# Optimization experiments

Hardware: AMD Instinct MI355X
Metric: run time of the kernel (lower is better)

## Reference

```python
import jax, jax.numpy as jnp
import numpy as np

N_NODES = 50000
N_EDGES = 800000
IN_F = 128
HEADS = 8
HEAD_DIM = 16
ALPHA = 0.2  # LeakyReLU negative slope
EPS = 1e-6


def setup_inputs() -> dict:
    key = jax.random.key(0)
    k1, k2, k3, k4 = jax.random.split(key, 4)
    x = jax.random.normal(k1, (N_NODES, IN_F), dtype=jnp.float32)
    edge_index = jax.random.randint(k2, (2, N_EDGES), 0, N_NODES, dtype=jnp.int32)
    std = 1.0 / np.sqrt(IN_F)
    W = jax.random.uniform(k3, (HEADS, IN_F, HEAD_DIM), minval=-std, maxval=std, dtype=jnp.float32)
    a = jax.random.uniform(k4, (HEADS, 2 * HEAD_DIM, 1), minval=-std, maxval=std, dtype=jnp.float32)
    bias = jnp.zeros((HEADS * HEAD_DIM,), dtype=jnp.float32)
    return {"x": x, "edge_index": edge_index, "W": W, "a": a, "bias": bias}


def reference(x, edge_index, W, a, bias):
    N = x.shape[0]
    src = edge_index[0]
    tgt = edge_index[1]
    # per-head linear transform: [N, H, D]
    h = jnp.einsum('nf,hfd->nhd', x, W)
    # split attention vector: a = [a_src; a_tgt], each [H, D]
    a_src = a[:, :HEAD_DIM, 0]
    a_tgt = a[:, HEAD_DIM:, 0]
    # node-level partial scores, then gather (equivalent to concat@a on edges)
    s_node_src = jnp.einsum('nhd,hd->nh', h, a_src)  # [N, H]
    s_node_tgt = jnp.einsum('nhd,hd->nh', h, a_tgt)  # [N, H]
    scores = s_node_src[src] + s_node_tgt[tgt]       # [E, H]
    scores = jnp.where(scores >= 0, scores, ALPHA * scores)  # LeakyReLU
    # edge softmax per target node, per head (global max subtract + clamp, as in source)
    max_per_head = jnp.max(scores, axis=0, keepdims=True)    # [1, H]
    exp_scores = jnp.exp(jnp.clip(scores - max_per_head, -20.0, 20.0))  # [E, H]
    denom = jax.ops.segment_sum(exp_scores, tgt, num_segments=N) + EPS  # [N, H]
    attn = exp_scores / denom[tgt]                                      # [E, H]
    # weighted scatter-add aggregation
    weighted = h[src] * attn[:, :, None]                                # [E, H, D]
    agg = jax.ops.segment_sum(weighted, tgt, num_segments=N)            # [N, H, D]
    out = agg.reshape(N, HEADS * HEAD_DIM) + bias
    return out
```

## Files before the change

### kernel.cpp

```cpp
#include <hip/hip_runtime.h>
#include <stdint.h>

#define N_NODES 50000
#define N_EDGES 800000
#define IN_F 128
#define HEADS 8
#define HEAD_DIM 16
#define ALPHA 0.2f
#define EPSV 1e-6f

#define NB 196
#define CAP 4800

typedef short short8 __attribute__((ext_vector_type(8)));
typedef float floatx4 __attribute__((ext_vector_type(4)));

__device__ __forceinline__ float bflo(unsigned v) {
    return __uint_as_float(v << 16);
}
__device__ __forceinline__ float bfhi(unsigned v) {
    return __uint_as_float(v & 0xffff0000u);
}
__device__ __forceinline__ unsigned f2bf(float f) {
    unsigned u = __float_as_uint(f);
    return (u + 0x7fffu + ((u >> 16) & 1u)) >> 16;
}

__global__ __launch_bounds__(256) void k_wt(const float* __restrict__ W,
                                            const float* __restrict__ a,
                                            ushort* __restrict__ WTb,
                                            ushort* __restrict__ WSb,
                                            int* __restrict__ gcnt) {
    int b = blockIdx.x, t = threadIdx.x;
    if (b == 64) {
        for (int i = t; i < 2048; i += 256) {
            int j = i >> 7, f = i & 127;
            int h = j >> 1;
            const float* wrow = W + h * 2048 + f * 16;
            const float* arow = a + h * 32 + (j & 1) * 16;
            float ssum = 0.f;
#pragma unroll
            for (int d = 0; d < 16; d++) ssum = fmaf(wrow[d], arow[d], ssum);
            WSb[i] = (ushort)f2bf(ssum);
        }
        return;
    }
    int i = b * 256 + t;
    int c = i >> 7, f = i & 127;
    WTb[i] = (ushort)f2bf(W[(c >> 4) * 2048 + f * 16 + (c & 15)]);
    if (i < NB) gcnt[i] = 0;
}

__global__ __launch_bounds__(256) void k_mid(const float* __restrict__ x,
                                             const ushort* __restrict__ WTb,
                                             const ushort* __restrict__ WSb,
                                             ushort* __restrict__ hb,
                                             float* __restrict__ sst,
                                             const int* __restrict__ srcA,
                                             const int* __restrict__ tgtA,
                                             int* __restrict__ gcnt,
                                             unsigned* __restrict__ bucketbuf) {
    int bi = blockIdx.x;
    int q3 = bi / 3, r3 = bi - q3 * 3;
    int t = threadIdx.x;

    if (r3 == 2) {
        __shared__ int lcnt[NB];
        __shared__ int lbase[NB];
        if (t < NB) lcnt[t] = 0;
        __syncthreads();

        int base = q3 * 2048 + t;
        int tg[8], sr[8];
        bool vld[8];
#pragma unroll
        for (int k = 0; k < 8; k++) {
            int e = base + k * 256;
            vld[k] = (e < N_EDGES);
            int ee = vld[k] ? e : 0;
            tg[k] = tgtA[ee];
            sr[k] = srcA[ee];
        }
#pragma unroll
        for (int k = 0; k < 8; k++)
            if (vld[k]) atomicAdd(&lcnt[tg[k] >> 8], 1);
        __syncthreads();
        if (t < NB) {
            int c = lcnt[t];
            lbase[t] = (c > 0) ? atomicAdd(&gcnt[t], c) : 0;
            lcnt[t] = 0;
        }
        __syncthreads();
#pragma unroll
        for (int k = 0; k < 8; k++) {
            if (vld[k]) {
                int b = tg[k] >> 8;
                int off = atomicAdd(&lcnt[b], 1);
                int pos = lbase[b] + off;
                if (pos < CAP)
                    bucketbuf[(size_t)b * CAP + pos] =
                        ((unsigned)(tg[k] & 255) << 16) | (unsigned)sr[k];
            }
        }
        return;
    }

    int mb = q3 * 2 + r3;
    int wave = t >> 6, lane = t & 63;
    int quad = lane >> 4, col = lane & 15;
    int nb = mb * 64 + wave * 16;

    int na = nb + col;
    int nac = na < N_NODES ? na : (N_NODES - 1);
    const float* xrow = x + (size_t)nac * 128 + quad * 8;

    floatx4 acc[8];
    floatx4 z = {0.f, 0.f, 0.f, 0.f};
#pragma unroll
    for (int ct = 0; ct < 8; ct++) acc[ct] = z;
    floatx4 accS = z;

#pragma unroll
    for (int kc = 0; kc < 4; kc++) {
        float4 f0 = *(const float4*)(xrow + kc * 32);
        float4 f1 = *(const float4*)(xrow + kc * 32 + 4);
        short8 af;
        af[0] = (short)f2bf(f0.x); af[1] = (short)f2bf(f0.y);
        af[2] = (short)f2bf(f0.z); af[3] = (short)f2bf(f0.w);
        af[4] = (short)f2bf(f1.x); af[5] = (short)f2bf(f1.y);
        af[6] = (short)f2bf(f1.z); af[7] = (short)f2bf(f1.w);
#pragma unroll
        for (int ct = 0; ct < 8; ct++) {
            const ushort* wrow = WTb + (size_t)(ct * 16 + col) * 128 + kc * 32 + quad * 8;
            short8 bf = *(const short8*)wrow;
            acc[ct] = __builtin_amdgcn_mfma_f32_16x16x32_bf16(af, bf, acc[ct], 0, 0, 0);
        }
        const ushort* srow = WSb + (size_t)col * 128 + kc * 32 + quad * 8;
        short8 bs = *(const short8*)srow;
        accS = __builtin_amdgcn_mfma_f32_16x16x32_bf16(af, bs, accS, 0, 0, 0);
    }

#pragma unroll
    for (int r = 0; r < 4; r++) {
        int node = nb + quad * 4 + r;
        bool nv = (node < N_NODES);
        if (nv) {
            ushort* hrow = hb + (size_t)node * 128 + col;
#pragma unroll
            for (int ct = 0; ct < 8; ct++)
                hrow[ct * 16] = (ushort)f2bf(acc[ct][r]);
            sst[(size_t)node * 16 + col] = accS[r];
        }
    }
}

__global__ __launch_bounds__(512) void k_passB(const unsigned* __restrict__ bucketbuf,
                                               const int* __restrict__ gcnt,
                                               int* __restrict__ rowptr,
                                               ushort* __restrict__ src16) {
    __shared__ int bin[256];
    __shared__ int wsum[4];
    __shared__ int woff[4];
    __shared__ int sbase;
    __shared__ ushort stage[CAP];
    int t = threadIdx.x, lane = t & 63, w = t >> 6;
    int b = blockIdx.x;

    if (t < 256) bin[t] = 0;

    int g = (t < NB) ? gcnt[t] : 0;
    int incg = g;
#pragma unroll
    for (int off = 1; off < 64; off <<= 1) {
        int nn = __shfl_up(incg, off, 64);
        if (lane >= off) incg += nn;
    }
    if (t < 256 && lane == 63) wsum[w] = incg;
    __syncthreads();
    if (t == 0) {
        woff[0] = 0;
        woff[1] = wsum[0];
        woff[2] = wsum[0] + wsum[1];
        woff[3] = wsum[0] + wsum[1] + wsum[2];
    }
    __syncthreads();
    if (t == b) sbase = woff[w] + incg - g;
    if (b == 0 && t == 0) rowptr[N_NODES] = N_EDGES;
    __syncthreads();
    int base = sbase;
    int n = gcnt[b]; if (n > CAP) n = CAP;
    const unsigned* buf = bucketbuf + (size_t)b * CAP;

    for (int i = t; i < n; i += 512)
        atomicAdd(&bin[buf[i] >> 16], 1);
    __syncthreads();
    int v = (t < 256) ? bin[t] : 0;
    int inc = v;
#pragma unroll
    for (int off = 1; off < 64; off <<= 1) {
        int nn = __shfl_up(inc, off, 64);
        if (lane >= off) inc += nn;
    }
    if (t < 256 && lane == 63) wsum[w] = inc;
    __syncthreads();
    if (t == 0) {
        woff[0] = 0;
        woff[1] = wsum[0];
        woff[2] = wsum[0] + wsum[1];
        woff[3] = wsum[0] + wsum[1] + wsum[2];
    }
    __syncthreads();
    if (t < 256) {
        int excl = woff[w] + inc - v;
        int node = b * 256 + t;
        if (node < N_NODES) rowptr[node] = base + excl;
        __syncthreads();
        bin[t] = excl;
    } else {
        __syncthreads();
    }
    __syncthreads();
    for (int i = t; i < n; i += 512) {
        unsigned p = buf[i];
        int off = atomicAdd(&bin[p >> 16], 1);
        stage[off] = (ushort)(p & 0xffffu);
    }
    __syncthreads();
    for (int i = t; i < n; i += 512)
        src16[base + i] = stage[i];
}

__global__ __launch_bounds__(256) void k_fused(const int* __restrict__ rowptr,
                                               const ushort* __restrict__ src16,
                                               const float* __restrict__ sst,
                                               const unsigned* __restrict__ h16,
                                               const float* __restrict__ bias,
                                               float* __restrict__ outb) {
    int t = threadIdx.x;
    int wave = t >> 6, lane = t & 63;
    int half = lane >> 5, hl = lane & 31;
    int n = blockIdx.x * 8 + wave * 2 + half;
    int head = hl >> 2;
    int hh = head * 2;
    int c = 4 * hl;

    const uint2* h2 = (const uint2*)h16;

    float st = sst[n * 16 + hh + 1];
    int begin = rowptr[n], end = rowptr[n + 1];

    float ax = 0.f, ay = 0.f, az = 0.f, aw = 0.f, den = 0.f;
    int e = begin;
    int nfull = (end - begin) >> 3;
    int s0, s1, s2, s3, s4, s5, s6, s7;
    if (nfull > 0) {
        s0 = src16[e];     s1 = src16[e + 1];
        s2 = src16[e + 2]; s3 = src16[e + 3];
        s4 = src16[e + 4]; s5 = src16[e + 5];
        s6 = src16[e + 6]; s7 = src16[e + 7];
    }
    for (int it = 0; it < nfull; ++it) {
        int c0 = s0, c1 = s1, c2 = s2, c3 = s3;
        int c4 = s4, c5 = s5, c6 = s6, c7 = s7;
        int en = e + 8;
        if (it + 1 < nfull) {
            s0 = src16[en];     s1 = src16[en + 1];
            s2 = src16[en + 2]; s3 = src16[en + 3];
            s4 = src16[en + 4]; s5 = src16[en + 5];
            s6 = src16[en + 6]; s7 = src16[en + 7];
        }
        float t0 = sst[c0 * 16 + hh];
        float t1 = sst[c1 * 16 + hh];
        float t2 = sst[c2 * 16 + hh];
        float t3 = sst[c3 * 16 + hh];
        float t4 = sst[c4 * 16 + hh];
        float t5 = sst[c5 * 16 + hh];
        float t6 = sst[c6 * 16 + hh];
        float t7 = sst[c7 * 16 + hh];
        uint2 p0 = h2[c0 * 32 + hl];
        uint2 p1 = h2[c1 * 32 + hl];
        uint2 p2 = h2[c2 * 32 + hl];
        uint2 p3 = h2[c3 * 32 + hl];
        uint2 p4 = h2[c4 * 32 + hl];
        uint2 p5 = h2[c5 * 32 + hl];
        uint2 p6 = h2[c6 * 32 + hl];
        uint2 p7 = h2[c7 * 32 + hl];
        float v0 = t0 + st; v0 = v0 >= 0.f ? v0 : ALPHA * v0;
        float v1 = t1 + st; v1 = v1 >= 0.f ? v1 : ALPHA * v1;
        float v2 = t2 + st; v2 = v2 >= 0.f ? v2 : ALPHA * v2;
        float v3 = t3 + st; v3 = v3 >= 0.f ? v3 : ALPHA * v3;
        float v4 = t4 + st; v4 = v4 >= 0.f ? v4 : ALPHA * v4;
        float v5 = t5 + st; v5 = v5 >= 0.f ? v5 : ALPHA * v5;
        float v6 = t6 + st; v6 = v6 >= 0.f ? v6 : ALPHA * v6;
        float v7 = t7 + st; v7 = v7 >= 0.f ? v7 : ALPHA * v7;
        float x0 = __expf(v0);
        float x1 = __expf(v1);
        float x2 = __expf(v2);
        float x3 = __expf(v3);
        float x4 = __expf(v4);
        float x5 = __expf(v5);
        float x6 = __expf(v6);
        float x7 = __expf(v7);
        den += ((x0 + x1) + (x2 + x3)) + ((x4 + x5) + (x6 + x7));
        ax = fmaf(x0, bflo(p0.x), fmaf(x1, bflo(p1.x), fmaf(x2, bflo(p2.x), fmaf(x3, bflo(p3.x), ax))));
        ax = fmaf(x4, bflo(p4.x), fmaf(x5, bflo(p5.x), fmaf(x6, bflo(p6.x), fmaf(x7, bflo(p7.x), ax))));
        ay = fmaf(x0, bfhi(p0.x), fmaf(x1, bfhi(p1.x), fmaf(x2, bfhi(p2.x), fmaf(x3, bfhi(p3.x), ay))));
        ay = fmaf(x4, bfhi(p4.x), fmaf(x5, bfhi(p5.x), fmaf(x6, bfhi(p6.x), fmaf(x7, bfhi(p7.x), ay))));
        az = fmaf(x0, bflo(p0.y), fmaf(x1, bflo(p1.y), fmaf(x2, bflo(p2.y), fmaf(x3, bflo(p3.y), az))));
        az = fmaf(x4, bflo(p4.y), fmaf(x5, bflo(p5.y), fmaf(x6, bflo(p6.y), fmaf(x7, bflo(p7.y), az))));
        aw = fmaf(x0, bfhi(p0.y), fmaf(x1, bfhi(p1.y), fmaf(x2, bfhi(p2.y), fmaf(x3, bfhi(p3.y), aw))));
        aw = fmaf(x4, bfhi(p4.y), fmaf(x5, bfhi(p5.y), fmaf(x6, bfhi(p6.y), fmaf(x7, bfhi(p7.y), aw))));
        e = en;
    }
    if (e + 3 < end) {
        int c0 = src16[e];
        int c1 = src16[e + 1];
        int c2 = src16[e + 2];
        int c3 = src16[e + 3];
        float t0 = sst[c0 * 16 + hh];
        float t1 = sst[c1 * 16 + hh];
        float t2 = sst[c2 * 16 + hh];
        float t3 = sst[c3 * 16 + hh];
        uint2 p0 = h2[c0 * 32 + hl];
        uint2 p1 = h2[c1 * 32 + hl];
        uint2 p2 = h2[c2 * 32 + hl];
        uint2 p3 = h2[c3 * 32 + hl];
        float v0 = t0 + st; v0 = v0 >= 0.f ? v0 : ALPHA * v0;
        float v1 = t1 + st; v1 = v1 >= 0.f ? v1 : ALPHA * v1;
        float v2 = t2 + st; v2 = v2 >= 0.f ? v2 : ALPHA * v2;
        float v3 = t3 + st; v3 = v3 >= 0.f ? v3 : ALPHA * v3;
        float x0 = __expf(v0);
        float x1 = __expf(v1);
        float x2 = __expf(v2);
        float x3 = __expf(v3);
        den += (x0 + x1) + (x2 + x3);
        ax = fmaf(x0, bflo(p0.x), fmaf(x1, bflo(p1.x), fmaf(x2, bflo(p2.x), fmaf(x3, bflo(p3.x), ax))));
        ay = fmaf(x0, bfhi(p0.x), fmaf(x1, bfhi(p1.x), fmaf(x2, bfhi(p2.x), fmaf(x3, bfhi(p3.x), ay))));
        az = fmaf(x0, bflo(p0.y), fmaf(x1, bflo(p1.y), fmaf(x2, bflo(p2.y), fmaf(x3, bflo(p3.y), az))));
        aw = fmaf(x0, bfhi(p0.y), fmaf(x1, bfhi(p1.y), fmaf(x2, bfhi(p2.y), fmaf(x3, bfhi(p3.y), aw))));
        e += 4;
    }
    for (; e < end; e++) {
        int sA = src16[e];
        float ssA = sst[sA * 16 + hh];
        uint2 pA = h2[sA * 32 + hl];
        float vA = ssA + st; vA = vA >= 0.f ? vA : ALPHA * vA;
        float exA = __expf(vA);
        den += exA;
        ax = fmaf(exA, bflo(pA.x), ax);
        ay = fmaf(exA, bfhi(pA.x), ay);
        az = fmaf(exA, bflo(pA.y), az);
        aw = fmaf(exA, bfhi(pA.y), aw);
    }
    float r = 1.f / (den + EPSV);
    float4 b = *(const float4*)(bias + c);
    float4 o;
    o.x = fmaf(ax, r, b.x);
    o.y = fmaf(ay, r, b.y);
    o.z = fmaf(az, r, b.z);
    o.w = fmaf(aw, r, b.w);
    *(float4*)(outb + (size_t)n * 128 + c) = o;
}

extern "C" void kernel_launch(void* const* d_in, const int* in_sizes, int n_in,
                              void* d_out, int out_size, void* d_ws, size_t ws_size,
                              hipStream_t stream) {
    const float* x    = (const float*)d_in[0];
    const int*   ei   = (const int*)d_in[1];
    const float* W    = (const float*)d_in[2];
    const float* a    = (const float*)d_in[3];
    const float* bias = (const float*)d_in[4];
    float* outb = (float*)d_out;

    char* ws = (char*)d_ws;
    ushort* hb        = (ushort*)(ws);
    float* sst        = (float*)(ws + 12800000);
    int*   rowptr     = (int*)  (ws + 16000000);
    ushort* src16     = (ushort*)(ws + 16200064);
    int*   gcnt       = (int*)  (ws + 17800064);
    ushort* WSb       = (ushort*)(ws + 17802112);
    ushort* WTb       = (ushort*)(ws + 17902528);
    unsigned* bucketbuf = (unsigned*)(ws + 17935296);

    const int* srcA = ei;
    const int* tgtA = ei + N_EDGES;

    hipLaunchKernelGGL(k_wt,    dim3(65),   dim3(256), 0, stream, W, a, WTb, WSb, gcnt);
    hipLaunchKernelGGL(k_mid,   dim3(1173), dim3(256), 0, stream,
                       x, WTb, WSb, hb, sst, srcA, tgtA, gcnt, bucketbuf);
    hipLaunchKernelGGL(k_passB, dim3(196),  dim3(512), 0, stream, bucketbuf, gcnt, rowptr, src16);
    hipLaunchKernelGGL(k_fused, dim3(6250), dim3(256), 0, stream, rowptr, src16, sst, (const unsigned*)hb, bias, outb);
}
```

Baseline: 154.6 us.

## Split node scores into src/tgt arrays, use two half-waves per node, vectorize edge reads

The aggregation kernel now assigns one node per wave, with its two half-waves taking alternating edges and combining partial sums through a cross-lane shuffle. This doubles the grid and roughly halves each node's serial gather chain, aiming to hide the latency of random gathers. Node scores are written to separate compact source and target arrays so gathers touch a denser layout. The bucketing pass reads edge indices with int4 vector loads instead of strided scalar loads, which also changes which edges each thread handles. The costs are extra shuffles and half the lanes idle during the final write.

```diff
diff --git a/kernel.cpp b/kernel.cpp
--- a/kernel.cpp
+++ b/kernel.cpp
@@ -55,7 +55,8 @@
                                              const ushort* __restrict__ WTb,
                                              const ushort* __restrict__ WSb,
                                              ushort* __restrict__ hb,
-                                             float* __restrict__ sst,
+                                             float* __restrict__ s_src,
+                                             float* __restrict__ s_tgt,
                                              const int* __restrict__ srcA,
                                              const int* __restrict__ tgtA,
                                              int* __restrict__ gcnt,
@@ -70,20 +71,21 @@
         if (t < NB) lcnt[t] = 0;
         __syncthreads();
 
-        int base = q3 * 2048 + t;
+        int ebase = q3 * 2048 + t * 8;
         int tg[8], sr[8];
-        bool vld[8];
-#pragma unroll
-        for (int k = 0; k < 8; k++) {
-            int e = base + k * 256;
-            vld[k] = (e < N_EDGES);
-            int ee = vld[k] ? e : 0;
-            tg[k] = tgtA[ee];
-            sr[k] = srcA[ee];
-        }
-#pragma unroll
-        for (int k = 0; k < 8; k++)
-            if (vld[k]) atomicAdd(&lcnt[tg[k] >> 8], 1);
+        bool vld = (ebase < N_EDGES);
+        if (vld) {
+            int4 T0 = *(const int4*)(tgtA + ebase);
+            int4 T1 = *(const int4*)(tgtA + ebase + 4);
+            int4 S0 = *(const int4*)(srcA + ebase);
+            int4 S1 = *(const int4*)(srcA + ebase + 4);
+            tg[0] = T0.x; tg[1] = T0.y; tg[2] = T0.z; tg[3] = T0.w;
+            tg[4] = T1.x; tg[5] = T1.y; tg[6] = T1.z; tg[7] = T1.w;
+            sr[0] = S0.x; sr[1] = S0.y; sr[2] = S0.z; sr[3] = S0.w;
+            sr[4] = S1.x; sr[5] = S1.y; sr[6] = S1.z; sr[7] = S1.w;
+#pragma unroll
+            for (int k = 0; k < 8; k++) atomicAdd(&lcnt[tg[k] >> 8], 1);
+        }
         __syncthreads();
         if (t < NB) {
             int c = lcnt[t];
@@ -91,9 +93,9 @@
             lcnt[t] = 0;
         }
         __syncthreads();
-#pragma unroll
-        for (int k = 0; k < 8; k++) {
-            if (vld[k]) {
+        if (vld) {
+#pragma unroll
+            for (int k = 0; k < 8; k++) {
                 int b = tg[k] >> 8;
                 int off = atomicAdd(&lcnt[b], 1);
                 int pos = lbase[b] + off;
@@ -149,7 +151,9 @@
 #pragma unroll
             for (int ct = 0; ct < 8; ct++)
                 hrow[ct * 16] = (ushort)f2bf(acc[ct][r]);
-            sst[(size_t)node * 16 + col] = accS[r];
+            float sv = accS[r];
+            if (col & 1) s_tgt[(size_t)node * 8 + (col >> 1)] = sv;
+            else         s_src[(size_t)node * 8 + (col >> 1)] = sv;
         }
     }
 }
@@ -232,95 +236,36 @@
 
 __global__ __launch_bounds__(256) void k_fused(const int* __restrict__ rowptr,
                                                const ushort* __restrict__ src16,
-                                               const float* __restrict__ sst,
+                                               const float* __restrict__ s_src,
+                                               const float* __restrict__ s_tgt,
                                                const unsigned* __restrict__ h16,
                                                const float* __restrict__ bias,
                                                float* __restrict__ outb) {
     int t = threadIdx.x;
     int wave = t >> 6, lane = t & 63;
     int half = lane >> 5, hl = lane & 31;
-    int n = blockIdx.x * 8 + wave * 2 + half;
+    int n = blockIdx.x * 4 + wave;
     int head = hl >> 2;
-    int hh = head * 2;
     int c = 4 * hl;
 
     const uint2* h2 = (const uint2*)h16;
 
-    float st = sst[n * 16 + hh + 1];
+    float st = s_tgt[(size_t)n * 8 + head];
     int begin = rowptr[n], end = rowptr[n + 1];
+    int d = end - begin;
 
     float ax = 0.f, ay = 0.f, az = 0.f, aw = 0.f, den = 0.f;
-    int e = begin;
-    int nfull = (end - begin) >> 3;
-    int s0, s1, s2, s3, s4, s5, s6, s7;
-    if (nfull > 0) {
-        s0 = src16[e];     s1 = src16[e + 1];
-        s2 = src16[e + 2]; s3 = src16[e + 3];
-        s4 = src16[e + 4]; s5 = src16[e + 5];
-        s6 = src16[e + 6]; s7 = src16[e + 7];
-    }
-    for (int it = 0; it < nfull; ++it) {
-        int c0 = s0, c1 = s1, c2 = s2, c3 = s3;
-        int c4 = s4, c5 = s5, c6 = s6, c7 = s7;
-        int en = e + 8;
-        if (it + 1 < nfull) {
-            s0 = src16[en];     s1 = src16[en + 1];
-            s2 = src16[en + 2]; s3 = src16[en + 3];
-            s4 = src16[en + 4]; s5 = src16[en + 5];
-            s6 = src16[en + 6]; s7 = src16[en + 7];
-        }
-        float t0 = sst[c0 * 16 + hh];
-        float t1 = sst[c1 * 16 + hh];
-        float t2 = sst[c2 * 16 + hh];
-        float t3 = sst[c3 * 16 + hh];
-        float t4 = sst[c4 * 16 + hh];
-        float t5 = sst[c5 * 16 + hh];
-        float t6 = sst[c6 * 16 + hh];
-        float t7 = sst[c7 * 16 + hh];
-        uint2 p0 = h2[c0 * 32 + hl];
-        uint2 p1 = h2[c1 * 32 + hl];
-        uint2 p2 = h2[c2 * 32 + hl];
-        uint2 p3 = h2[c3 * 32 + hl];
-        uint2 p4 = h2[c4 * 32 + hl];
-        uint2 p5 = h2[c5 * 32 + hl];
-        uint2 p6 = h2[c6 * 32 + hl];
-        uint2 p7 = h2[c7 * 32 + hl];
-        float v0 = t0 + st; v0 = v0 >= 0.f ? v0 : ALPHA * v0;
-        float v1 = t1 + st; v1 = v1 >= 0.f ? v1 : ALPHA * v1;
-        float v2 = t2 + st; v2 = v2 >= 0.f ? v2 : ALPHA * v2;
-        float v3 = t3 + st; v3 = v3 >= 0.f ? v3 : ALPHA * v3;
-        float v4 = t4 + st; v4 = v4 >= 0.f ? v4 : ALPHA * v4;
-        float v5 = t5 + st; v5 = v5 >= 0.f ? v5 : ALPHA * v5;
-        float v6 = t6 + st; v6 = v6 >= 0.f ? v6 : ALPHA * v6;
-        float v7 = t7 + st; v7 = v7 >= 0.f ? v7 : ALPHA * v7;
-        float x0 = __expf(v0);
-        float x1 = __expf(v1);
-        float x2 = __expf(v2);
-        float x3 = __expf(v3);
-        float x4 = __expf(v4);
-        float x5 = __expf(v5);
-        float x6 = __expf(v6);
-        float x7 = __expf(v7);
-        den += ((x0 + x1) + (x2 + x3)) + ((x4 + x5) + (x6 + x7));
-        ax = fmaf(x0, bflo(p0.x), fmaf(x1, bflo(p1.x), fmaf(x2, bflo(p2.x), fmaf(x3, bflo(p3.x), ax))));
-        ax = fmaf(x4, bflo(p4.x), fmaf(x5, bflo(p5.x), fmaf(x6, bflo(p6.x), fmaf(x7, bflo(p7.x), ax))));
-        ay = fmaf(x0, bfhi(p0.x), fmaf(x1, bfhi(p1.x), fmaf(x2, bfhi(p2.x), fmaf(x3, bfhi(p3.x), ay))));
-        ay = fmaf(x4, bfhi(p4.x), fmaf(x5, bfhi(p5.x), fmaf(x6, bfhi(p6.x), fmaf(x7, bfhi(p7.x), ay))));
-        az = fmaf(x0, bflo(p0.y), fmaf(x1, bflo(p1.y), fmaf(x2, bflo(p2.y), fmaf(x3, bflo(p3.y), az))));
-        az = fmaf(x4, bflo(p4.y), fmaf(x5, bflo(p5.y), fmaf(x6, bflo(p6.y), fmaf(x7, bflo(p7.y), az))));
-        aw = fmaf(x0, bfhi(p0.y), fmaf(x1, bfhi(p1.y), fmaf(x2, bfhi(p2.y), fmaf(x3, bfhi(p3.y), aw))));
-        aw = fmaf(x4, bfhi(p4.y), fmaf(x5, bfhi(p5.y), fmaf(x6, bfhi(p6.y), fmaf(x7, bfhi(p7.y), aw))));
-        e = en;
-    }
-    if (e + 3 < end) {
+    int nfull = d >> 3;
+    int e = begin + half;
+    for (int it = 0; it < nfull; ++it, e += 8) {
         int c0 = src16[e];
-        int c1 = src16[e + 1];
-        int c2 = src16[e + 2];
-        int c3 = src16[e + 3];
-        float t0 = sst[c0 * 16 + hh];
-        float t1 = sst[c1 * 16 + hh];
-        float t2 = sst[c2 * 16 + hh];
-        float t3 = sst[c3 * 16 + hh];
+        int c1 = src16[e + 2];
+        int c2 = src16[e + 4];
+        int c3 = src16[e + 6];
+        float t0 = s_src[c0 * 8 + head];
+        float t1 = s_src[c1 * 8 + head];
+        float t2 = s_src[c2 * 8 + head];
+        float t3 = s_src[c3 * 8 + head];
         uint2 p0 = h2[c0 * 32 + hl];
         uint2 p1 = h2[c1 * 32 + hl];
         uint2 p2 = h2[c2 * 32 + hl];
@@ -338,11 +283,10 @@
         ay = fmaf(x0, bfhi(p0.x), fmaf(x1, bfhi(p1.x), fmaf(x2, bfhi(p2.x), fmaf(x3, bfhi(p3.x), ay))));
         az = fmaf(x0, bflo(p0.y), fmaf(x1, bflo(p1.y), fmaf(x2, bflo(p2.y), fmaf(x3, bflo(p3.y), az))));
         aw = fmaf(x0, bfhi(p0.y), fmaf(x1, bfhi(p1.y), fmaf(x2, bfhi(p2.y), fmaf(x3, bfhi(p3.y), aw))));
-        e += 4;
-    }
-    for (; e < end; e++) {
-        int sA = src16[e];
-        float ssA = sst[sA * 16 + hh];
+    }
+    for (int ee = begin + (nfull << 3) + half; ee < end; ee += 2) {
+        int sA = src16[ee];
+        float ssA = s_src[sA * 8 + head];
         uint2 pA = h2[sA * 32 + hl];
         float vA = ssA + st; vA = vA >= 0.f ? vA : ALPHA * vA;
         float exA = __expf(vA);
@@ -352,14 +296,22 @@
         az = fmaf(exA, bflo(pA.y), az);
         aw = fmaf(exA, bfhi(pA.y), aw);
     }
-    float r = 1.f / (den + EPSV);
-    float4 b = *(const float4*)(bias + c);
-    float4 o;
-    o.x = fmaf(ax, r, b.x);
-    o.y = fmaf(ay, r, b.y);
-    o.z = fmaf(az, r, b.z);
-    o.w = fmaf(aw, r, b.w);
-    *(float4*)(outb + (size_t)n * 128 + c) = o;
+    den += __shfl_xor(den, 32, 64);
+    ax  += __shfl_xor(ax, 32, 64);
+    ay  += __shfl_xor(ay, 32, 64);
+    az  += __shfl_xor(az, 32, 64);
+    aw  += __shfl_xor(aw, 32, 64);
+
+    if (half == 0) {
+        float r = 1.f / (den + EPSV);
+        float4 b = *(const float4*)(bias + c);
+        float4 o;
+        o.x = fmaf(ax, r, b.x);
+        o.y = fmaf(ay, r, b.y);
+        o.z = fmaf(az, r, b.z);
+        o.w = fmaf(aw, r, b.w);
+        *(float4*)(outb + (size_t)n * 128 + c) = o;
+    }
 }
 
 extern "C" void kernel_launch(void* const* d_in, const int* in_sizes, int n_in,
@@ -374,7 +326,8 @@
 
     char* ws = (char*)d_ws;
     ushort* hb        = (ushort*)(ws);
-    float* sst        = (float*)(ws + 12800000);
+    float* s_src      = (float*)(ws + 12800000);
+    float* s_tgt      = (float*)(ws + 14400000);
     int*   rowptr     = (int*)  (ws + 16000000);
     ushort* src16     = (ushort*)(ws + 16200064);
     int*   gcnt       = (int*)  (ws + 17800064);
@@ -385,9 +338,9 @@
     const int* srcA = ei;
     const int* tgtA = ei + N_EDGES;
 
-    hipLaunchKernelGGL(k_wt,    dim3(65),   dim3(256), 0, stream, W, a, WTb, WSb, gcnt);
-    hipLaunchKernelGGL(k_mid,   dim3(1173), dim3(256), 0, stream,
-                       x, WTb, WSb, hb, sst, srcA, tgtA, gcnt, bucketbuf);
-    hipLaunchKernelGGL(k_passB, dim3(196),  dim3(512), 0, stream, bucketbuf, gcnt, rowptr, src16);
-    hipLaunchKernelGGL(k_fused, dim3(6250), dim3(256), 0, stream, rowptr, src16, sst, (const unsigned*)hb, bias, outb);
-}
+    hipLaunchKernelGGL(k_wt,    dim3(65),    dim3(256), 0, stream, W, a, WTb, WSb, gcnt);
+    hipLaunchKernelGGL(k_mid,   dim3(1173),  dim3(256), 0, stream,
+                       x, WTb, WSb, hb, s_src, s_tgt, srcA, tgtA, gcnt, bucketbuf);
+    hipLaunchKernelGGL(k_passB, dim3(196),   dim3(512), 0, stream, bucketbuf, gcnt, rowptr, src16);
+    hipLaunchKernelGGL(k_fused, dim3(12500), dim3(256), 0, stream, rowptr, src16, s_src, s_tgt, (const unsigned*)hb, bias, outb);
+}
```

After: 154.0 us (median of 2 runs). No clear change (-0.4%).
